# Kernel optimization log

Hardware: AMD Instinct MI355X
Metric: run time of the kernel (lower is better)

Reference implementation:

```python
import jax, jax.numpy as jnp
import numpy as np

B, C, U, LEN, K = 32, 16, 16, 128, 4  # batch, channels, units, image side, cheb order
POWERS = K + 1


def _path_chebyshev(n, k):
    """Chebyshev polynomials T_0..T_k of the rescaled normalized Laplacian of an
    undirected path graph with n nodes. Returns [k+1, n, n] float32."""
    A = np.zeros((n, n), dtype=np.float64)
    A[np.arange(n - 1), np.arange(1, n)] = 1.0
    A = A + A.T
    d = A.sum(axis=1)
    dinv = 1.0 / np.sqrt(d)
    L = np.eye(n) - dinv[:, None] * A * dinv[None, :]   # normalized Laplacian
    Lt = L - np.eye(n)                                   # rescaled: 2L/lambda_max - I, lambda_max=2
    T = [np.eye(n), Lt]
    for _ in range(2, k + 1):
        T.append(2.0 * Lt @ T[-1] - T[-2])
    return np.stack(T[: k + 1]).astype(np.float32)


def setup_inputs() -> dict:
    key = jax.random.key(0)
    kx, kc = jax.random.split(key)
    x = jax.random.normal(kx, (B, C, LEN, LEN), dtype=jnp.float32)
    coefs = 0.001 * jax.random.normal(kc, (POWERS, POWERS, C, U), dtype=jnp.float32)
    cheb = jnp.asarray(_path_chebyshev(LEN, K))  # same graph for both axes
    return {"x": x, "coefs": coefs, "cheb1": cheb, "cheb2": cheb}


def reference(x, coefs, cheb1, cheb2):
    # out[b,u,p,q] = sum_{k1,k2,c,h,w} coefs[k1,k2,c,u] * cheb1[k1,h,p] * x[b,c,h,w] * cheb2[k2,w,q]
    t1 = jnp.einsum('bchw,khp->bkcpw', x, cheb1)        # apply cheb1 along H
    s = jnp.einsum('bkcpw,klcu->blupw', t1, coefs)      # contract k1 and channels
    out = jnp.einsum('blupw,lwq->bupq', s, cheb2)       # apply cheb2 along W, contract k2
    return out
```

## Files before the change

### kernel.cpp

```cpp
#include <hip/hip_runtime.h>
#include <hip/hip_bf16.h>

#define LEN 128
#define NB 32
#define NC 16
#define NU 16
#define NK 5
#define KC 80
#define KCP 96

typedef unsigned int uint32;
typedef unsigned short ushort16;
typedef __attribute__((ext_vector_type(8))) short bf16x8;
typedef __attribute__((ext_vector_type(4))) float f32x4;

#define MFMA(a, b, c) __builtin_amdgcn_mfma_f32_16x16x32_bf16(a, b, c, 0, 0, 0)

#define SIG(r) (((r) & 15) ^ (((r) >> 3) & 15))

static __device__ inline ushort16 f2bf(float f) {
    union { float f; uint32 u; } v; v.f = f;
    uint32 u = v.u;
    uint32 r = (u + 0x7fffu + ((u >> 16) & 1u)) >> 16;
    return (ushort16)r;
}
static __device__ inline uint32 pkbf(float a, float b) {
    return (uint32)f2bf(a) | ((uint32)f2bf(b) << 16);
}
static __device__ inline bf16x8 frag16(const void* p) {
    return *(const bf16x8*)p;
}

__global__ __launch_bounds__(256) void k0_prep(const float* __restrict__ coefs,
                                               const float* __restrict__ cheb1,
                                               const float* __restrict__ cheb2,
                                               ushort16* __restrict__ cheb1F,
                                               ushort16* __restrict__ cheb2F,
                                               ushort16* __restrict__ coefF) {
    int i = blockIdx.x * 256 + threadIdx.x;
    if (i < 81920) {
        int j = i & 7, lane = (i >> 3) & 63, ks = (i >> 9) & 3, nt = i >> 11;
        int kp = nt * 16 + (lane & 15);
        int k = kp >> 7, p = kp & 127;
        int h = ks * 32 + ((lane >> 4) << 3) + j;
        cheb1F[i] = f2bf(cheb1[(k * LEN + h) * LEN + p]);
    } else if (i < 163840) {
        int i2 = i - 81920;
        int j = i2 & 7, lane = (i2 >> 3) & 63, t = i2 >> 9;
        int ks = t % 20, nt = t / 20;
        int q = nt * 16 + (lane & 15);
        int lw = ks * 32 + ((lane >> 4) << 3) + j;
        int l = lw >> 7, w = lw & 127;
        cheb2F[i2] = f2bf(cheb2[(l * LEN + w) * LEN + q]);
    } else if (i < 171520) {
        int i3 = i - 163840;
        int j = i3 & 7, lane = (i3 >> 3) & 63, t = i3 >> 9;
        int ks = t % 3, nt = t / 3;
        int lu = nt * 16 + (lane & 15);
        int l = lu >> 4, u = lu & 15;
        int kc = ks * 32 + ((lane >> 4) << 3) + j;
        int k = kc >> 4, c = kc & 15;
        coefF[i3] = (kc < KC) ? f2bf(coefs[((k * NK + l) * NC + c) * NU + u]) : (ushort16)0;
    }
}

__global__ __launch_bounds__(256) void kx_prep(const float* __restrict__ x,
                                               ushort16* __restrict__ xF) {
    __shared__ __align__(16) uint32 Xs[128 * 64];
    const int bc = blockIdx.x;
    const int tid = threadIdx.x;
    const float* xp = x + (size_t)bc * (LEN * LEN);
    {
        int w = tid & 127, hg = tid >> 7;
        #pragma unroll
        for (int uu = 0; uu < 8; ++uu) {
            int u = hg * 8 + uu;
            uint4 d;
            uint32* dp = (uint32*)&d;
            #pragma unroll
            for (int t = 0; t < 4; ++t) {
                int h2 = u * 4 + t;
                dp[t] = pkbf(xp[(2 * h2) * LEN + w], xp[(2 * h2 + 1) * LEN + w]);
            }
            *(uint4*)(Xs + w * 64 + ((u ^ SIG(w)) << 2)) = d;
        }
    }
    __syncthreads();
    ushort16* dst = xF + (size_t)bc * 16384;
    #pragma unroll
    for (int i = 0; i < 8; ++i) {
        int n = tid + i * 256;
        int lane = n & 63, fk = n >> 6;
        int wrow = (fk >> 2) * 16 + (lane & 15);
        int u = (fk & 3) * 4 + (lane >> 4);
        uint4 v = *(const uint4*)(Xs + wrow * 64 + ((u ^ SIG(wrow)) << 2));
        *(uint4*)(dst + (size_t)n * 8) = v;
    }
}

__global__ __launch_bounds__(256, 4) void k1_mfma(const ushort16* __restrict__ xF,
                                                  const ushort16* __restrict__ cheb1F,
                                                  ushort16* __restrict__ t1, int b0) {
    __shared__ __align__(16) uint32 Bs[80 * 64];
    const int c = blockIdx.x, bl = blockIdx.y, ns = blockIdx.z;
    const int b = b0 + bl;
    const int tid = threadIdx.x;
    const int lane = tid & 63, wm = tid >> 6;
    const int m16 = lane & 15, g = lane >> 4;

    const ushort16* xFb = xF + ((size_t)(b * NC + c)) * 16384;

    f32x4 acc[2][5];
    #pragma unroll
    for (int mi = 0; mi < 2; ++mi)
        #pragma unroll
        for (int ni = 0; ni < 5; ++ni) acc[mi][ni] = (f32x4)0.f;

    #pragma unroll
    for (int ks = 0; ks < 4; ++ks) {
        bf16x8 Af[2], Bf[5];
        #pragma unroll
        for (int mi = 0; mi < 2; ++mi) {
            int mt = wm * 2 + mi;
            Af[mi] = frag16(xFb + ((size_t)(mt * 4 + ks) * 64 + lane) * 8);
        }
        #pragma unroll
        for (int ni = 0; ni < 5; ++ni) {
            int nt = ns * 5 + ni;
            Bf[ni] = frag16(cheb1F + ((size_t)(nt * 4 + ks) * 64 + lane) * 8);
        }
        #pragma unroll
        for (int mi = 0; mi < 2; ++mi)
            #pragma unroll
            for (int ni = 0; ni < 5; ++ni)
                acc[mi][ni] = MFMA(Af[mi], Bf[ni], acc[mi][ni]);
    }

    #pragma unroll
    for (int ni = 0; ni < 5; ++ni)
        #pragma unroll
        for (int mi = 0; mi < 2; ++mi) {
            int rr = ni * 16 + m16;
            int wu = wm * 32 + mi * 16 + g * 4;
            uint2 d;
            d.x = pkbf(acc[mi][ni][0], acc[mi][ni][1]);
            d.y = pkbf(acc[mi][ni][2], acc[mi][ni][3]);
            int u = wu >> 3;
            *(uint2*)(Bs + rr * 64 + ((u ^ SIG(rr)) << 2) + ((wu >> 1) & 3)) = d;
        }
    __syncthreads();

    #pragma unroll
    for (int i = 0; i < 5; ++i) {
        int n = tid + i * 256;
        int rr = n >> 4, wsg = n & 15;
        uint4 v = *(const uint4*)(Bs + rr * 64 + ((wsg ^ SIG(rr)) << 2));
        int kp = ns * 80 + rr;
        int k = kp >> 7, p = kp & 127;
        *(uint4*)(t1 + ((size_t)((bl * LEN + p) * KC + k * NC + c)) * LEN + wsg * 8) = v;
    }
}

__global__ __launch_bounds__(256, 4) void k2_mfma(const ushort16* __restrict__ t1,
                                                  const ushort16* __restrict__ coefF,
                                                  const ushort16* __restrict__ cheb2F,
                                                  float* __restrict__ out, int b0) {
    __shared__ __align__(16) uint32 sm[128 * 64];
    const int p = blockIdx.x, bl = blockIdx.y, b = b0 + bl;
    const int tid = threadIdx.x;
    const int lane = tid & 63, wave = tid >> 6;
    const int n16 = lane & 15, g = lane >> 4;

    {
        const uint32* t1u = (const uint32*)(t1 + (size_t)(bl * LEN + p) * (KC * LEN));
        #pragma unroll
        for (int i = 0; i < 3; ++i) {
            int it = tid + i * 256;
            if (it < 640) {
                int a = it >> 4, wq = it & 15;
                const uint32* src = t1u + (2 * a) * 64 + wq * 4;
                uint4 Av = *(const uint4*)(src);
                uint4 Bv = *(const uint4*)(src + 64);
                const uint32* av = (const uint32*)&Av;
                const uint32* bv = (const uint32*)&Bv;
                int u = a >> 2, lo = a & 3;
                #pragma unroll
                for (int j = 0; j < 4; ++j) {
                    int r0 = wq * 8 + 2 * j, r1 = r0 + 1;
                    sm[r0 * 64 + ((u ^ SIG(r0)) << 2) + lo] = (av[j] & 0xffffu) | (bv[j] << 16);
                    sm[r1 * 64 + ((u ^ SIG(r1)) << 2) + lo] = (av[j] >> 16) | (bv[j] & 0xffff0000u);
                }
            }
        }
        #pragma unroll
        for (int i = 0; i < 4; ++i) {
            int idx = tid + i * 256;
            int row = idx >> 3, d = idx & 7;
            int u = 10 + (d >> 2);
            sm[row * 64 + ((u ^ SIG(row)) << 2) + (d & 3)] = 0;
        }
    }
    __syncthreads();

    f32x4 acc[2][5];
    #pragma unroll
    for (int mi = 0; mi < 2; ++mi)
        #pragma unroll
        for (int ni = 0; ni < 5; ++ni) acc[mi][ni] = (f32x4)0.f;

    #pragma unroll
    for (int ks = 0; ks < 3; ++ks) {
        bf16x8 Af[2], Bf[5];
        #pragma unroll
        for (int mi = 0; mi < 2; ++mi) {
            int row = wave * 32 + mi * 16 + n16;
            int uu = ks * 4 + g;
            Af[mi] = frag16(sm + row * 64 + ((uu ^ SIG(row)) << 2));
        }
        #pragma unroll
        for (int ni = 0; ni < 5; ++ni)
            Bf[ni] = frag16(coefF + ((size_t)(ni * 3 + ks) * 64 + lane) * 8);
        #pragma unroll
        for (int mi = 0; mi < 2; ++mi)
            #pragma unroll
            for (int ni = 0; ni < 5; ++ni)
                acc[mi][ni] = MFMA(Af[mi], Bf[ni], acc[mi][ni]);
    }
    __syncthreads();

    {
        ushort16* A3 = (ushort16*)sm;
        #pragma unroll
        for (int mi = 0; mi < 2; ++mi)
            #pragma unroll
            for (int ni = 0; ni < 5; ++ni) {
                int wcol = wave * 32 + mi * 16 + g * 4;
                uint2 d;
                d.x = pkbf(acc[mi][ni][0], acc[mi][ni][1]);
                d.y = pkbf(acc[mi][ni][2], acc[mi][ni][3]);
                *(uint2*)(A3 + n16 * 648 + ni * 128 + wcol) = d;
            }
    }
    __syncthreads();

    const ushort16* A3r = (const ushort16*)sm;
    f32x4 c3[2];
    c3[0] = (f32x4)0.f; c3[1] = (f32x4)0.f;
    #pragma unroll 5
    for (int ks = 0; ks < 20; ++ks) {
        bf16x8 Aa = frag16(A3r + n16 * 648 + ks * 32 + g * 8);
        #pragma unroll
        for (int nt = 0; nt < 2; ++nt) {
            bf16x8 Bb = frag16(cheb2F + ((size_t)((wave * 2 + nt) * 20 + ks) * 64 + lane) * 8);
            c3[nt] = MFMA(Aa, Bb, c3[nt]);
        }
    }

    #pragma unroll
    for (int nt = 0; nt < 2; ++nt)
        #pragma unroll
        for (int r = 0; r < 4; ++r) {
            int u = g * 4 + r;
            int q = wave * 32 + nt * 16 + n16;
            out[(((size_t)(b * NU + u)) * LEN + p) * LEN + q] = c3[nt][r];
        }
}

extern "C" void kernel_launch(void* const* d_in, const int* in_sizes, int n_in,
                              void* d_out, int out_size, void* d_ws, size_t ws_size,
                              hipStream_t stream) {
    const float* x     = (const float*)d_in[0];
    const float* coefs = (const float*)d_in[1];
    const float* cheb1 = (const float*)d_in[2];
    const float* cheb2 = (const float*)d_in[3];
    float* out = (float*)d_out;

    const size_t xF_bytes  = (size_t)NB * NC * 16384 * sizeof(ushort16);
    const size_t aux_bytes = 163840 + 163840 + 15360;
    size_t off = (ws_size - aux_bytes - xF_bytes) & ~(size_t)255;
    ushort16* cheb1F = (ushort16*)((char*)d_ws + off);
    ushort16* cheb2F = cheb1F + 81920;
    ushort16* coefF  = cheb2F + 81920;
    ushort16* xF     = coefF + 7680;
    ushort16* t1 = (ushort16*)d_ws;

    const size_t per_b = (size_t)LEN * KC * LEN * sizeof(ushort16);
    int chunk = (int)(off / per_b);
    if (chunk < 1) chunk = 1;
    if (chunk > NB) chunk = NB;

    hipLaunchKernelGGL(k0_prep, dim3(171520 / 256), dim3(256), 0, stream,
                       coefs, cheb1, cheb2, cheb1F, cheb2F, coefF);
    hipLaunchKernelGGL(kx_prep, dim3(NB * NC), dim3(256), 0, stream, x, xF);
    for (int b0 = 0; b0 < NB; b0 += chunk) {
        int cb = (NB - b0 < chunk) ? (NB - b0) : chunk;
        hipLaunchKernelGGL(k1_mfma, dim3(NC, cb, 8), dim3(256), 0, stream,
                           xF, cheb1F, t1, b0);
        hipLaunchKernelGGL(k2_mfma, dim3(LEN, cb), dim3(256), 0, stream,
                           t1, coefF, cheb2F, out, b0);
    }
}
```

Before: 151.0 us.

## Merge prep kernels, raise occupancy bound, batch t1 loads before LDS stores

Folds the coefficient/Chebyshev prep kernel and the x-layout prep kernel into one launch, with block ranges split by index, to save a kernel launch. It raises the launch-bounds occupancy hint from 4 to 5 blocks per SM on both MFMA kernels. It also restructures k2's t1 staging so every global load is issued first and the LDS zero-fill and scatter follow. The changes trade register pressure for overlap, and the higher occupancy target may force register spills.

```diff
diff --git a/kernel.cpp b/kernel.cpp
--- a/kernel.cpp
+++ b/kernel.cpp
@@ -31,74 +31,75 @@
     return *(const bf16x8*)p;
 }
 
-__global__ __launch_bounds__(256) void k0_prep(const float* __restrict__ coefs,
-                                               const float* __restrict__ cheb1,
-                                               const float* __restrict__ cheb2,
-                                               ushort16* __restrict__ cheb1F,
-                                               ushort16* __restrict__ cheb2F,
-                                               ushort16* __restrict__ coefF) {
-    int i = blockIdx.x * 256 + threadIdx.x;
-    if (i < 81920) {
-        int j = i & 7, lane = (i >> 3) & 63, ks = (i >> 9) & 3, nt = i >> 11;
-        int kp = nt * 16 + (lane & 15);
-        int k = kp >> 7, p = kp & 127;
-        int h = ks * 32 + ((lane >> 4) << 3) + j;
-        cheb1F[i] = f2bf(cheb1[(k * LEN + h) * LEN + p]);
-    } else if (i < 163840) {
-        int i2 = i - 81920;
-        int j = i2 & 7, lane = (i2 >> 3) & 63, t = i2 >> 9;
-        int ks = t % 20, nt = t / 20;
-        int q = nt * 16 + (lane & 15);
-        int lw = ks * 32 + ((lane >> 4) << 3) + j;
-        int l = lw >> 7, w = lw & 127;
-        cheb2F[i2] = f2bf(cheb2[(l * LEN + w) * LEN + q]);
-    } else if (i < 171520) {
-        int i3 = i - 163840;
-        int j = i3 & 7, lane = (i3 >> 3) & 63, t = i3 >> 9;
-        int ks = t % 3, nt = t / 3;
-        int lu = nt * 16 + (lane & 15);
-        int l = lu >> 4, u = lu & 15;
-        int kc = ks * 32 + ((lane >> 4) << 3) + j;
-        int k = kc >> 4, c = kc & 15;
-        coefF[i3] = (kc < KC) ? f2bf(coefs[((k * NK + l) * NC + c) * NU + u]) : (ushort16)0;
-    }
-}
-
-__global__ __launch_bounds__(256) void kx_prep(const float* __restrict__ x,
-                                               ushort16* __restrict__ xF) {
+__global__ __launch_bounds__(256) void kprep(const float* __restrict__ x,
+                                             const float* __restrict__ coefs,
+                                             const float* __restrict__ cheb1,
+                                             const float* __restrict__ cheb2,
+                                             ushort16* __restrict__ xF,
+                                             ushort16* __restrict__ cheb1F,
+                                             ushort16* __restrict__ cheb2F,
+                                             ushort16* __restrict__ coefF) {
     __shared__ __align__(16) uint32 Xs[128 * 64];
-    const int bc = blockIdx.x;
-    const int tid = threadIdx.x;
-    const float* xp = x + (size_t)bc * (LEN * LEN);
-    {
-        int w = tid & 127, hg = tid >> 7;
-        #pragma unroll
-        for (int uu = 0; uu < 8; ++uu) {
-            int u = hg * 8 + uu;
-            uint4 d;
-            uint32* dp = (uint32*)&d;
-            #pragma unroll
-            for (int t = 0; t < 4; ++t) {
-                int h2 = u * 4 + t;
-                dp[t] = pkbf(xp[(2 * h2) * LEN + w], xp[(2 * h2 + 1) * LEN + w]);
+    const int blk = blockIdx.x, tid = threadIdx.x;
+    if (blk < 512) {
+        const int bc = blk;
+        const float* xp = x + (size_t)bc * (LEN * LEN);
+        {
+            int w = tid & 127, hg = tid >> 7;
+            #pragma unroll
+            for (int uu = 0; uu < 8; ++uu) {
+                int u = hg * 8 + uu;
+                uint4 d;
+                uint32* dp = (uint32*)&d;
+                #pragma unroll
+                for (int t = 0; t < 4; ++t) {
+                    int h2 = u * 4 + t;
+                    dp[t] = pkbf(xp[(2 * h2) * LEN + w], xp[(2 * h2 + 1) * LEN + w]);
+                }
+                *(uint4*)(Xs + w * 64 + ((u ^ SIG(w)) << 2)) = d;
             }
-            *(uint4*)(Xs + w * 64 + ((u ^ SIG(w)) << 2)) = d;
-        }
-    }
-    __syncthreads();
-    ushort16* dst = xF + (size_t)bc * 16384;
-    #pragma unroll
-    for (int i = 0; i < 8; ++i) {
-        int n = tid + i * 256;
-        int lane = n & 63, fk = n >> 6;
-        int wrow = (fk >> 2) * 16 + (lane & 15);
-        int u = (fk & 3) * 4 + (lane >> 4);
-        uint4 v = *(const uint4*)(Xs + wrow * 64 + ((u ^ SIG(wrow)) << 2));
-        *(uint4*)(dst + (size_t)n * 8) = v;
-    }
-}
-
-__global__ __launch_bounds__(256, 4) void k1_mfma(const ushort16* __restrict__ xF,
+        }
+        __syncthreads();
+        ushort16* dst = xF + (size_t)bc * 16384;
+        #pragma unroll
+        for (int i = 0; i < 8; ++i) {
+            int n = tid + i * 256;
+            int lane = n & 63, fk = n >> 6;
+            int wrow = (fk >> 2) * 16 + (lane & 15);
+            int u = (fk & 3) * 4 + (lane >> 4);
+            uint4 v = *(const uint4*)(Xs + wrow * 64 + ((u ^ SIG(wrow)) << 2));
+            *(uint4*)(dst + (size_t)n * 8) = v;
+        }
+    } else {
+        int i = (blk - 512) * 256 + tid;
+        if (i < 81920) {
+            int j = i & 7, lane = (i >> 3) & 63, ks = (i >> 9) & 3, nt = i >> 11;
+            int kp = nt * 16 + (lane & 15);
+            int k = kp >> 7, p = kp & 127;
+            int h = ks * 32 + ((lane >> 4) << 3) + j;
+            cheb1F[i] = f2bf(cheb1[(k * LEN + h) * LEN + p]);
+        } else if (i < 163840) {
+            int i2 = i - 81920;
+            int j = i2 & 7, lane = (i2 >> 3) & 63, t = i2 >> 9;
+            int ks = t % 20, nt = t / 20;
+            int q = nt * 16 + (lane & 15);
+            int lw = ks * 32 + ((lane >> 4) << 3) + j;
+            int l = lw >> 7, w = lw & 127;
+            cheb2F[i2] = f2bf(cheb2[(l * LEN + w) * LEN + q]);
+        } else {
+            int i3 = i - 163840;
+            int j = i3 & 7, lane = (i3 >> 3) & 63, t = i3 >> 9;
+            int ks = t % 3, nt = t / 3;
+            int lu = nt * 16 + (lane & 15);
+            int l = lu >> 4, u = lu & 15;
+            int kc = ks * 32 + ((lane >> 4) << 3) + j;
+            int k = kc >> 4, c = kc & 15;
+            coefF[i3] = (kc < KC) ? f2bf(coefs[((k * NK + l) * NC + c) * NU + u]) : (ushort16)0;
+        }
+    }
+}
+
+__global__ __launch_bounds__(256, 5) void k1_mfma(const ushort16* __restrict__ xF,
                                                   const ushort16* __restrict__ cheb1F,
                                                   ushort16* __restrict__ t1, int b0) {
     __shared__ __align__(16) uint32 Bs[80 * 64];
@@ -161,7 +162,7 @@
     }
 }
 
-__global__ __launch_bounds__(256, 4) void k2_mfma(const ushort16* __restrict__ t1,
+__global__ __launch_bounds__(256, 5) void k2_mfma(const ushort16* __restrict__ t1,
                                                   const ushort16* __restrict__ coefF,
                                                   const ushort16* __restrict__ cheb2F,
                                                   float* __restrict__ out, int b0) {
@@ -171,33 +172,39 @@
     const int lane = tid & 63, wave = tid >> 6;
     const int n16 = lane & 15, g = lane >> 4;
 
-    {
-        const uint32* t1u = (const uint32*)(t1 + (size_t)(bl * LEN + p) * (KC * LEN));
-        #pragma unroll
-        for (int i = 0; i < 3; ++i) {
-            int it = tid + i * 256;
-            if (it < 640) {
-                int a = it >> 4, wq = it & 15;
-                const uint32* src = t1u + (2 * a) * 64 + wq * 4;
-                uint4 Av = *(const uint4*)(src);
-                uint4 Bv = *(const uint4*)(src + 64);
-                const uint32* av = (const uint32*)&Av;
-                const uint32* bv = (const uint32*)&Bv;
-                int u = a >> 2, lo = a & 3;
-                #pragma unroll
-                for (int j = 0; j < 4; ++j) {
-                    int r0 = wq * 8 + 2 * j, r1 = r0 + 1;
-                    sm[r0 * 64 + ((u ^ SIG(r0)) << 2) + lo] = (av[j] & 0xffffu) | (bv[j] << 16);
-                    sm[r1 * 64 + ((u ^ SIG(r1)) << 2) + lo] = (av[j] >> 16) | (bv[j] & 0xffff0000u);
-                }
+    const uint32* t1u = (const uint32*)(t1 + (size_t)(bl * LEN + p) * (KC * LEN));
+    uint4 Av[3], Bv[3];
+    #pragma unroll
+    for (int i = 0; i < 3; ++i) {
+        int it = tid + i * 256;
+        if (it < 640) {
+            int a2 = it >> 4, wq = it & 15;
+            const uint32* src = t1u + a2 * 128 + wq * 4;
+            Av[i] = *(const uint4*)(src);
+            Bv[i] = *(const uint4*)(src + 64);
+        }
+    }
+    #pragma unroll
+    for (int i = 0; i < 4; ++i) {
+        int idx = tid + i * 256;
+        int row = idx >> 3, d = idx & 7;
+        int u = 10 + (d >> 2);
+        sm[row * 64 + ((u ^ SIG(row)) << 2) + (d & 3)] = 0;
+    }
+    #pragma unroll
+    for (int i = 0; i < 3; ++i) {
+        int it = tid + i * 256;
+        if (it < 640) {
+            int a2 = it >> 4, wq = it & 15;
+            const uint32* av = (const uint32*)&Av[i];
+            const uint32* bv = (const uint32*)&Bv[i];
+            int u = a2 >> 2, lo = a2 & 3;
+            #pragma unroll
+            for (int j = 0; j < 4; ++j) {
+                int r0 = wq * 8 + 2 * j, r1 = r0 + 1;
+                sm[r0 * 64 + ((u ^ SIG(r0)) << 2) + lo] = (av[j] & 0xffffu) | (bv[j] << 16);
+                sm[r1 * 64 + ((u ^ SIG(r1)) << 2) + lo] = (av[j] >> 16) | (bv[j] & 0xffff0000u);
             }
-        }
-        #pragma unroll
-        for (int i = 0; i < 4; ++i) {
-            int idx = tid + i * 256;
-            int row = idx >> 3, d = idx & 7;
-            int u = 10 + (d >> 2);
-            sm[row * 64 + ((u ^ SIG(row)) << 2) + (d & 3)] = 0;
         }
     }
     __syncthreads();
@@ -214,8 +221,7 @@
         #pragma unroll
         for (int mi = 0; mi < 2; ++mi) {
             int row = wave * 32 + mi * 16 + n16;
-            int uu = ks * 4 + g;
-            Af[mi] = frag16(sm + row * 64 + ((uu ^ SIG(row)) << 2));
+            Af[mi] = frag16(sm + row * 64 + (((ks * 4 + g) ^ SIG(row)) << 2));
         }
         #pragma unroll
         for (int ni = 0; ni < 5; ++ni)
@@ -289,9 +295,8 @@
     if (chunk < 1) chunk = 1;
     if (chunk > NB) chunk = NB;
 
-    hipLaunchKernelGGL(k0_prep, dim3(171520 / 256), dim3(256), 0, stream,
-                       coefs, cheb1, cheb2, cheb1F, cheb2F, coefF);
-    hipLaunchKernelGGL(kx_prep, dim3(NB * NC), dim3(256), 0, stream, x, xF);
+    hipLaunchKernelGGL(kprep, dim3(1182), dim3(256), 0, stream,
+                       x, coefs, cheb1, cheb2, xF, cheb1F, cheb2F, coefF);
     for (int b0 = 0; b0 < NB; b0 += chunk) {
         int cb = (NB - b0 < chunk) ? (NB - b0) : chunk;
         hipLaunchKernelGGL(k1_mfma, dim3(NC, cb, 8), dim3(256), 0, stream,
```

New measurement: 149.0 us. Within noise of the previous version (-1.3%).
